# Kernel tuning notes

Measured on AMD Instinct MI355X. Metric: run time of the kernel, lower is better.

## Reference

```python
import jax, jax.numpy as jnp
import numpy as np

B, S, D, E = 4, 2048, 1024, 8
HD = D // E          # per-expert head dim = 128
ROPE = HD // 2       # rotary dims = 64 (32 complex pairs)


def setup_inputs() -> dict:
    key = jax.random.key(0)
    ks = jax.random.split(key, 5)
    x = jax.random.normal(ks[0], (B, S, D), dtype=jnp.float32)
    Wg = jax.random.normal(ks[1], (D, E), dtype=jnp.float32) * 0.02
    Wqkv = jax.random.normal(ks[2], (E, D, 3 * HD), dtype=jnp.float32) * 0.02
    Wff = jax.random.normal(ks[3], (E, HD, D), dtype=jnp.float32) * 0.02
    b_ff = jnp.zeros((D,), dtype=jnp.float32)
    # precompute_freqs_cis(qk_rope_head_dim=ROPE, seqlen=S), theta=10000
    inv = 1.0 / (10000.0 ** (np.arange(0, ROPE, 2, dtype=np.float32) / ROPE))  # [ROPE//2]
    ang = np.arange(S, dtype=np.float32)[:, None] * inv[None, :]               # [S, ROPE//2]
    cos = jnp.asarray(np.cos(ang), dtype=jnp.float32)
    sin = jnp.asarray(np.sin(ang), dtype=jnp.float32)
    return {"x": x, "Wg": Wg, "Wqkv": Wqkv, "Wff": Wff, "b_ff": b_ff, "cos": cos, "sin": sin}


def _apply_rope(x, cos, sin):
    # x: [B,S,E,HD]; rotate the second half (x_pe), keep first half (x_nope), cat (pe, nope)
    b, s, e, hd = x.shape
    x_nope, x_pe = x[..., : hd // 2], x[..., hd // 2 :]
    xr = x_pe.reshape(b, s, e, hd // 4, 2)
    re, im = xr[..., 0], xr[..., 1]
    c = cos[None, :, None, :]
    sn = sin[None, :, None, :]
    rot = jnp.stack([re * c - im * sn, re * sn + im * c], axis=-1).reshape(b, s, e, hd // 2)
    return jnp.concatenate([rot, x_nope], axis=-1)


def reference(x, Wg, Wqkv, Wff, b_ff, cos, sin):
    b, s, d = x.shape
    e, hd = Wqkv.shape[0], Wqkv.shape[2] // 3
    # RoPE on per-expert chunks
    xh = _apply_rope(x.reshape(b, s, e, hd), cos, sin).reshape(b, s, d)
    # SwitchGate: top-1 routing
    probs = jax.nn.softmax(xh @ Wg, axis=-1)            # [b,s,E]
    expert = jnp.argmax(probs, axis=-1)                 # [b,s]
    gate = jnp.max(probs, axis=-1)                      # [b,s]
    # preprocess: per-expert stable gather of routed tokens (capacity = s, padded+masked)
    is_e = expert[None, :, :] == jnp.arange(e)[:, None, None]        # [E,b,s] bool
    order = jnp.argsort(jnp.where(is_e, 0, 1), axis=-1, stable=True)  # [E,b,s] routed-first
    mask_g = jnp.take_along_axis(is_e, order, axis=-1).astype(xh.dtype)  # [E,b,s]
    x_g = jnp.take_along_axis(xh[None], order[..., None], axis=2)    # [E,b,s,d]
    gate_g = jnp.take_along_axis(gate[None], order, axis=2)          # [E,b,s]
    # expert-grouped column-parallel QKV
    qkv = jnp.einsum("ebsd,edf->ebsf", x_g, Wqkv)                    # [E,b,s,3*hd]
    q, k, v = jnp.split(qkv, 3, axis=-1)                             # [E,b,s,hd]
    # grouped sparse attention within each expert's token set
    dot = jnp.einsum("ebqh,ebkh->ebqk", q, k) / jnp.sqrt(jnp.asarray(hd, xh.dtype))
    dot = dot - 1e6 * (1.0 - mask_g[:, :, None, :])
    attn = jax.nn.softmax(dot, axis=-1)
    ctx = jnp.einsum("ebqk,ebkh->ebqh", attn, v)                     # [E,b,s,hd]
    # row-parallel output projection, gate-weighted
    out = jnp.einsum("ebsh,ehd->ebsd", ctx, Wff) + b_ff
    out = out * (gate_g * mask_g)[..., None]
    # scatter_add combine back to [b,s,d]
    outs = jnp.zeros((b, s, d), dtype=xh.dtype)
    outs = outs.at[jnp.arange(b)[None, :, None], order].add(out)
    return outs
```

## Files before the change

kernel.cpp:

```cpp
#include <hip/hip_runtime.h>
#include <math.h>

#define Bn 4
#define Sn 2048
#define Dn 1024
#define En 8
#define HDn 128
#define NG 32
#define MAXT 160
#define MAXN 1024

typedef __attribute__((ext_vector_type(8))) short bf16x8;
typedef __attribute__((ext_vector_type(4))) float f32x4;
typedef unsigned short u16;

__device__ __forceinline__ unsigned bf16_rn(float x) {
  unsigned u = __float_as_uint(x);
  return (u + 0x7fffu + ((u >> 16) & 1u)) >> 16;
}
__device__ __forceinline__ void bsplit(float x, unsigned& hi, unsigned& lo) {
  hi = bf16_rn(x);
  lo = bf16_rn(x - __uint_as_float(hi << 16));
}
__device__ __forceinline__ void gl16(const void* g, void* l) {
  __builtin_amdgcn_global_load_lds(
      (const __attribute__((address_space(1))) void*)g,
      (__attribute__((address_space(3))) void*)l, 16, 0, 0);
}
#define MFMA16(a, b, c) __builtin_amdgcn_mfma_f32_16x16x32_bf16((a), (b), (c), 0, 0, 0)

__device__ __forceinline__ void prep_body(
    const float* __restrict__ W, u16* __restrict__ hiT, u16* __restrict__ loT,
    int Kdim, int Ndim, int e, int k0, int c0, float (*tile)[65])
{
  int t = threadIdx.x;
  int r = t >> 4, cc = (t & 15) << 2;
  const float* src = W + ((size_t)e * Kdim + k0) * Ndim + c0;
#pragma unroll
  for (int i = 0; i < 4; ++i) {
    float4 v = *(const float4*)(src + (size_t)(r + i * 16) * Ndim + cc);
    tile[r + i * 16][cc + 0] = v.x; tile[r + i * 16][cc + 1] = v.y;
    tile[r + i * 16][cc + 2] = v.z; tile[r + i * 16][cc + 3] = v.w;
  }
  __syncthreads();
#pragma unroll
  for (int i = 0; i < 4; ++i) {
    int oc = (t >> 4) + i * 16;
    int ok = (t & 15) << 2;
    float v0 = tile[ok + 0][oc], v1 = tile[ok + 1][oc];
    float v2 = tile[ok + 2][oc], v3 = tile[ok + 3][oc];
    unsigned h0,l0,h1,l1,h2,l2,h3,l3;
    bsplit(v0,h0,l0); bsplit(v1,h1,l1); bsplit(v2,h2,l2); bsplit(v3,h3,l3);
    size_t o = ((size_t)e * Ndim + c0 + oc) * Kdim + k0 + ok;
    *(ushort4*)(hiT + o) = make_ushort4((u16)h0,(u16)h1,(u16)h2,(u16)h3);
    *(ushort4*)(loT + o) = make_ushort4((u16)l0,(u16)l1,(u16)l2,(u16)l3);
  }
}

__global__ __launch_bounds__(256) void k_prologue(
    const float* __restrict__ x, const float* __restrict__ Wg,
    const float* __restrict__ cosT, const float* __restrict__ sinT,
    const float* __restrict__ Wqkv, const float* __restrict__ Wff,
    u16* __restrict__ xh_hi, u16* __restrict__ xh_lo,
    u16* __restrict__ WqT_hi, u16* __restrict__ WqT_lo,
    u16* __restrict__ WfT_hi, u16* __restrict__ WfT_lo,
    int* __restrict__ expertArr, float* __restrict__ gateArr,
    int* __restrict__ done)
{
  __shared__ float tile[64][65];
  int bid = blockIdx.x;
  if (bid == 0 && threadIdx.x == 0) done[0] = 0;
  if (bid < 2048) {
    int wid = threadIdx.x >> 6, l = threadIdx.x & 63;
    int bs = (bid << 2) + wid;
    int s  = bs & (Sn - 1);
    const float* xrow = x + (size_t)bs * Dn;
    float xa[8], xb[8];
#pragma unroll
    for (int d = 0; d < 8; ++d) {
      xa[d] = xrow[d * 128 + l];
      xb[d] = xrow[d * 128 + 64 + l];
    }
    float ce = cosT[s * 32 + (l >> 1)];
    float sn = sinT[s * 32 + (l >> 1)];
    float ve[8];
#pragma unroll
    for (int d = 0; d < 8; ++d) {
      float self = xb[d];
      float part = __shfl_xor(self, 1, 64);
      ve[d] = (l & 1) ? (part * sn + self * ce) : (self * ce - part * sn);
    }
    size_t obase = (size_t)bs * Dn + l;
#pragma unroll
    for (int d = 0; d < 8; ++d) {
      unsigned h0, l0, h1, l1;
      bsplit(ve[d], h0, l0);
      bsplit(xa[d], h1, l1);
      xh_hi[obase + d * 128]      = (u16)h0;
      xh_lo[obase + d * 128]      = (u16)l0;
      xh_hi[obase + d * 128 + 64] = (u16)h1;
      xh_lo[obase + d * 128 + 64] = (u16)l1;
    }

    float pl[8] = {0.f, 0.f, 0.f, 0.f, 0.f, 0.f, 0.f, 0.f};
#pragma unroll
    for (int d = 0; d < 8; ++d) {
      const float* w0 = Wg + (size_t)(d * 128 + l) * En;
      float4 wA = *(const float4*)w0;
      float4 wB = *(const float4*)(w0 + 4);
      float xv = ve[d];
      pl[0] += xv * wA.x; pl[1] += xv * wA.y; pl[2] += xv * wA.z; pl[3] += xv * wA.w;
      pl[4] += xv * wB.x; pl[5] += xv * wB.y; pl[6] += xv * wB.z; pl[7] += xv * wB.w;
      const float* w1 = Wg + (size_t)(d * 128 + 64 + l) * En;
      float4 wC = *(const float4*)w1;
      float4 wD = *(const float4*)(w1 + 4);
      xv = xa[d];
      pl[0] += xv * wC.x; pl[1] += xv * wC.y; pl[2] += xv * wC.z; pl[3] += xv * wC.w;
      pl[4] += xv * wD.x; pl[5] += xv * wD.y; pl[6] += xv * wD.z; pl[7] += xv * wD.w;
    }
#pragma unroll
    for (int off = 1; off < 64; off <<= 1) {
#pragma unroll
      for (int e = 0; e < 8; ++e) pl[e] += __shfl_xor(pl[e], off, 64);
    }
    float m = pl[0]; int be = 0;
#pragma unroll
    for (int e = 1; e < 8; ++e) if (pl[e] > m) { m = pl[e]; be = e; }
    float ss = 0.f;
#pragma unroll
    for (int e = 0; e < 8; ++e) ss += expf(pl[e] - m);
    if (l == 0) {
      expertArr[bs] = be;
      gateArr[bs] = 1.0f / ss;
    }
  } else if (bid < 2048 + 768) {
    int id = bid - 2048;
    int e = id / 96, r2 = id % 96;
    prep_body(Wqkv, WqT_hi, WqT_lo, Dn, 384, e, (r2 / 6) << 6, (r2 % 6) << 6, tile);
  } else {
    int id = bid - 2816;
    int e = id >> 5, r2 = id & 31;
    prep_body(Wff, WfT_hi, WfT_lo, HDn, Dn, e, (r2 >> 4) << 6, (r2 & 15) << 6, tile);
  }
}

__global__ __launch_bounds__(256) void k_route(
    const int* __restrict__ expertArr, int* __restrict__ idx, int* __restrict__ cnt,
    int* __restrict__ tileg, int* __restrict__ tilem, int* __restrict__ ntile,
    int* __restrict__ done)
{
  int g = blockIdx.x;
  int b = g >> 3, e = g & 7;
  int t = threadIdx.x;
  __shared__ int wtot[4];
  __shared__ int base;
  if (t == 0) base = 0;
  __syncthreads();
  for (int c = 0; c < Sn; c += 256) {
    int s = c + t;
    int pred = (expertArr[b * Sn + s] == e) ? 1 : 0;
    unsigned long long mask = __ballot(pred);
    int ln = t & 63, wv = t >> 6;
    int wpre = __popcll(mask & ((1ull << ln) - 1ull));
    if (ln == 63) wtot[wv] = wpre + pred;
    __syncthreads();
    int woff = 0;
    for (int w = 0; w < wv; ++w) woff += wtot[w];
    int tot = wtot[0] + wtot[1] + wtot[2] + wtot[3];
    if (pred) idx[(g << 11) + base + woff + wpre] = s;
    __syncthreads();
    if (t == 0) base += tot;
    __syncthreads();
  }
  if (t == 0) {
    cnt[g] = base;
    __threadfence();
    if (atomicAdd(done, 1) == NG - 1) {
      int tc = 0;
      for (int gg = 0; gg < NG; ++gg) {
        int nn = __hip_atomic_load(&cnt[gg], __ATOMIC_ACQUIRE, __HIP_MEMORY_SCOPE_AGENT);
        for (int m0 = 0; m0 < nn && tc < MAXT; m0 += 64) { tileg[tc] = gg; tilem[tc] = m0; ++tc; }
      }
      ntile[0] = tc;
    }
  }
}

__global__ __launch_bounds__(256) void k_qkv(
    const u16* __restrict__ xh_hi, const u16* __restrict__ xh_lo,
    const u16* __restrict__ WqT_hi, const u16* __restrict__ WqT_lo,
    const int* __restrict__ idx, const int* __restrict__ cnt,
    u16* __restrict__ qkv_hi, u16* __restrict__ qkv_lo,
    u16* __restrict__ vT_hi, u16* __restrict__ vT_lo)
{
  extern __shared__ unsigned char LDS[];
  int bid = blockIdx.x;
  int r8 = bid & 7, q = bid >> 3;
  int g = r8 + ((q & 3) << 3);
  int slot = q >> 2;
  int m0 = (slot >> 1) << 6;
  int n0 = (slot & 1) * 192;
  int n = cnt[g];
  if (m0 >= n) return;
  int b = g >> 3, e = g & 7;
  const int* idxg = idx + (g << 11);
  int t = threadIdx.x;
  int w = t >> 6, l = t & 63;
  int lc = l & 15, lq = l >> 4;

  int srow = t >> 2;
  int sslot = (t & 3) ^ ((srow >> 1) & 3);
  int rgs = m0 + srow; rgs = rgs < n ? rgs : n - 1;
  size_t aoffR = ((size_t)(b * Sn + idxg[rgs])) * Dn + sslot * 8;
  size_t boffR0 = ((size_t)e * 384 + n0 + srow) * Dn + sslot * 8;
  unsigned dst = (unsigned)t << 4;

  f32x4 acc[4][3];
#pragma unroll
  for (int i = 0; i < 4; ++i)
#pragma unroll
    for (int j = 0; j < 3; ++j) acc[i][j] = (f32x4){0.f, 0.f, 0.f, 0.f};

  unsigned off = (unsigned)((lq ^ ((lc >> 1) & 3)) << 4);

#define STAGE(bb, k0)                                                 \
  do {                                                                \
    gl16(xh_hi + aoffR + (k0), LDS + (bb) + dst);                     \
    gl16(xh_lo + aoffR + (k0), LDS + (bb) + 4096 + dst);              \
    gl16(WqT_hi + boffR0 + (k0), LDS + (bb) + 8192 + dst);            \
    gl16(WqT_hi + boffR0 + (size_t)64 * Dn + (k0), LDS + (bb) + 12288 + dst); \
    gl16(WqT_hi + boffR0 + (size_t)128 * Dn + (k0), LDS + (bb) + 16384 + dst);\
    gl16(WqT_lo + boffR0 + (k0), LDS + (bb) + 20480 + dst);           \
    gl16(WqT_lo + boffR0 + (size_t)64 * Dn + (k0), LDS + (bb) + 24576 + dst); \
    gl16(WqT_lo + boffR0 + (size_t)128 * Dn + (k0), LDS + (bb) + 28672 + dst);\
  } while (0)

  STAGE(0, 0);
  asm volatile("s_waitcnt vmcnt(0)" ::: "memory");
  __builtin_amdgcn_s_barrier();
  for (int tt = 0; tt < 32; ++tt) {
    unsigned cur = (tt & 1) ? 32768u : 0u;
    if (tt < 31) {
      STAGE(cur ^ 32768u, (tt + 1) * 32);
      asm volatile("s_waitcnt vmcnt(8)" ::: "memory");
    } else {
      asm volatile("s_waitcnt vmcnt(0)" ::: "memory");
    }
    __builtin_amdgcn_s_barrier();
    bf16x8 ah[4], al[4], bh[3], bl[3];
#pragma unroll
    for (int fi = 0; fi < 4; ++fi) {
      unsigned ab = cur + (unsigned)((fi * 16 + lc) * 64) + off;
      ah[fi] = *(const bf16x8*)(LDS + ab);
      al[fi] = *(const bf16x8*)(LDS + ab + 4096);
    }
#pragma unroll
    for (int fj = 0; fj < 3; ++fj) {
      unsigned bb2 = cur + 8192u + (unsigned)((w * 48 + fj * 16 + lc) * 64) + off;
      bh[fj] = *(const bf16x8*)(LDS + bb2);
      bl[fj] = *(const bf16x8*)(LDS + bb2 + 12288);
    }
    __builtin_amdgcn_s_setprio(1);
#pragma unroll
    for (int fi = 0; fi < 4; ++fi)
#pragma unroll
      for (int fj = 0; fj < 3; ++fj) {
        acc[fi][fj] = MFMA16(ah[fi], bh[fj], acc[fi][fj]);
        acc[fi][fj] = MFMA16(al[fi], bh[fj], acc[fi][fj]);
        acc[fi][fj] = MFMA16(ah[fi], bl[fj], acc[fi][fj]);
      }
    __builtin_amdgcn_s_setprio(0);
    asm volatile("s_waitcnt lgkmcnt(0)" ::: "memory");
    __builtin_amdgcn_sched_barrier(0);
    __builtin_amdgcn_s_barrier();
  }
#undef STAGE

#pragma unroll
  for (int fi = 0; fi < 4; ++fi) {
#pragma unroll
    for (int rr = 0; rr < 4; ++rr) {
      int rg = m0 + fi * 16 + lq * 4 + rr;
      if (rg < n) {
        int tok = idxg[rg];
#pragma unroll
        for (int fj = 0; fj < 3; ++fj) {
          int col = n0 + w * 48 + fj * 16 + lc;
          unsigned h, lo2;
          bsplit(acc[fi][fj][rr], h, lo2);
          if (col < 256) {
            size_t o = (size_t)(b * Sn + tok) * 384 + col;
            qkv_hi[o] = (u16)h; qkv_lo[o] = (u16)lo2;
          } else {
            size_t o = ((size_t)g * HDn + (col - 256)) * MAXN + rg;
            vT_hi[o] = (u16)h; vT_lo[o] = (u16)lo2;
          }
        }
      }
    }
  }
}

__global__ __launch_bounds__(256) void k_attn(
    const u16* __restrict__ qkv_hi, const u16* __restrict__ qkv_lo,
    const u16* __restrict__ vT_hi, const u16* __restrict__ vT_lo,
    const int* __restrict__ idx, const int* __restrict__ cnt,
    const int* __restrict__ tileg, const int* __restrict__ tilem,
    const int* __restrict__ ntile,
    u16* __restrict__ ctx_hi, u16* __restrict__ ctx_lo)
{
  extern __shared__ unsigned char LDS[];
  int tid = blockIdx.x;
  if (tid >= ntile[0]) return;
  int g = tileg[tid], m0 = tilem[tid];
  int n = cnt[g];
  int b = g >> 3;
  const int* idxg = idx + (g << 11);
  int t = threadIdx.x, wid = t >> 6, l = t & 63;
  int lc = l & 15, lq = l >> 4;
  const float scale = 0.08838834764831845f;

  int qrg = m0 + wid * 16 + lc; qrg = qrg < n ? qrg : n - 1;
  size_t qoff = (size_t)(b * Sn + idxg[qrg]) * 384 + lq * 8;
  bf16x8 Qhi[4], Qlo[4];
#pragma unroll
  for (int ks = 0; ks < 4; ++ks) {
    Qhi[ks] = *(const bf16x8*)(qkv_hi + qoff + ks * 32);
    Qlo[ks] = *(const bf16x8*)(qkv_lo + qoff + ks * 32);
  }

  f32x4 acc[8];
#pragma unroll
  for (int i = 0; i < 8; ++i) acc[i] = (f32x4){0.f, 0.f, 0.f, 0.f};
  float m_r[4] = {-1e30f, -1e30f, -1e30f, -1e30f};
  float l_r[4] = {0.f, 0.f, 0.f, 0.f};

  size_t vbase = ((size_t)g * HDn + lc) * MAXN + lq * 8;
  unsigned pbase = 65536u + wid * 4096u;

#define STAGEK(bufb, kc)                                                     \
  do {                                                                       \
    unsigned bb = (bufb);                                                    \
    for (int j = 0; j < 4; ++j) {                                            \
      int c = wid * 4 + j;                                                   \
      int row = (kc) + c * 4 + lq;                                           \
      int rg = row < n ? row : n - 1;                                        \
      int srcslot = lc ^ (((c & 1) << 2) | lq);                              \
      size_t soff = (size_t)(b * Sn + idxg[rg]) * 384 + 128 + srcslot * 8;   \
      gl16(qkv_hi + soff, LDS + bb + c * 1024);                              \
      gl16(qkv_lo + soff, LDS + bb + 16384 + c * 1024);                      \
    }                                                                        \
  } while (0)

  int nt = (n + 63) >> 6;
  STAGEK(0, 0);
  __syncthreads();

  for (int tt = 0; tt < nt; ++tt) {
    unsigned cur = (tt & 1) ? 32768u : 0u;
    if (tt + 1 < nt) STAGEK(cur ^ 32768u, (tt + 1) * 64);
    int kc = tt * 64;

    f32x4 Sf[4];
#pragma unroll
    for (int kf = 0; kf < 4; ++kf) Sf[kf] = (f32x4){0.f, 0.f, 0.f, 0.f};
    __builtin_amdgcn_s_setprio(1);
#pragma unroll
    for (int ks = 0; ks < 4; ++ks) {
#pragma unroll
      for (int kf = 0; kf < 4; ++kf) {
        int row = kf * 16 + lc;
        unsigned byte = cur + row * 256 + ((((ks << 2) | lq) ^ (row & 7)) << 4);
        bf16x8 kh = *(const bf16x8*)(LDS + byte);
        bf16x8 kl = *(const bf16x8*)(LDS + byte + 16384);
        Sf[kf] = MFMA16(Qhi[ks], kh, Sf[kf]);
        Sf[kf] = MFMA16(Qlo[ks], kh, Sf[kf]);
        Sf[kf] = MFMA16(Qhi[ks], kl, Sf[kf]);
      }
    }
    __builtin_amdgcn_s_setprio(0);

    float mloc[4] = {-1e30f, -1e30f, -1e30f, -1e30f};
#pragma unroll
    for (int kf = 0; kf < 4; ++kf) {
#pragma unroll
      for (int r = 0; r < 4; ++r) {
        int key = kc + kf * 16 + lc;
        float s = (key < n) ? Sf[kf][r] * scale : -1e30f;
        Sf[kf][r] = s;
        mloc[r] = fmaxf(mloc[r], s);
      }
    }
#pragma unroll
    for (int off = 1; off < 16; off <<= 1) {
#pragma unroll
      for (int r = 0; r < 4; ++r) mloc[r] = fmaxf(mloc[r], __shfl_xor(mloc[r], off, 64));
    }
    float corr[4], rs[4] = {0.f, 0.f, 0.f, 0.f};
#pragma unroll
    for (int r = 0; r < 4; ++r) {
      float mn = fmaxf(m_r[r], mloc[r]);
      corr[r] = expf(m_r[r] - mn);
      m_r[r] = mn;
    }
#pragma unroll
    for (int kf = 0; kf < 4; ++kf) {
#pragma unroll
      for (int r = 0; r < 4; ++r) {
        float p = expf(Sf[kf][r] - m_r[r]);
        rs[r] += p;
        unsigned ph, plo;
        bsplit(p, ph, plo);
        int prow = (lq << 2) | r;
        int slot = (kf << 1) | (lc >> 3);
        unsigned pb = pbase + prow * 128 + ((slot ^ (prow & 7)) << 4) + ((lc & 7) << 1);
        *(u16*)(LDS + pb) = (u16)ph;
        *(u16*)(LDS + pb + 2048) = (u16)plo;
      }
    }
#pragma unroll
    for (int off = 1; off < 16; off <<= 1) {
#pragma unroll
      for (int r = 0; r < 4; ++r) rs[r] += __shfl_xor(rs[r], off, 64);
    }
#pragma unroll
    for (int r = 0; r < 4; ++r) l_r[r] = l_r[r] * corr[r] + rs[r];
#pragma unroll
    for (int df = 0; df < 8; ++df)
#pragma unroll
      for (int r = 0; r < 4; ++r) acc[df][r] *= corr[r];

#pragma unroll
    for (int ks2 = 0; ks2 < 2; ++ks2) {
      unsigned pr = pbase + lc * 128 + ((((ks2 << 2) | lq) ^ (lc & 7)) << 4);
      bf16x8 pa = *(const bf16x8*)(LDS + pr);
      bf16x8 pl = *(const bf16x8*)(LDS + pr + 2048);
      __builtin_amdgcn_s_setprio(1);
#pragma unroll
      for (int df = 0; df < 8; ++df) {
        size_t vo = vbase + (size_t)(df * 16) * MAXN + kc + ks2 * 32;
        bf16x8 vh = *(const bf16x8*)(vT_hi + vo);
        bf16x8 vl = *(const bf16x8*)(vT_lo + vo);
        acc[df] = MFMA16(pa, vh, acc[df]);
        acc[df] = MFMA16(pl, vh, acc[df]);
        acc[df] = MFMA16(pa, vl, acc[df]);
      }
      __builtin_amdgcn_s_setprio(0);
    }
    __syncthreads();
  }
#undef STAGEK

#pragma unroll
  for (int r = 0; r < 4; ++r) {
    int rg = m0 + wid * 16 + (lq << 2) + r;
    if (rg < n) {
      int tok = idxg[rg];
      float inv = 1.0f / l_r[r];
      size_t o = (size_t)(b * Sn + tok) * HDn + lc;
#pragma unroll
      for (int df = 0; df < 8; ++df) {
        unsigned h, lo2;
        bsplit(acc[df][r] * inv, h, lo2);
        ctx_hi[o + df * 16] = (u16)h;
        ctx_lo[o + df * 16] = (u16)lo2;
      }
    }
  }
}

__global__ __launch_bounds__(256) void k_out(
    const u16* __restrict__ ctx_hi, const u16* __restrict__ ctx_lo,
    const u16* __restrict__ WfT_hi, const u16* __restrict__ WfT_lo,
    const float* __restrict__ bff,
    const int* __restrict__ idx, const int* __restrict__ cnt,
    const int* __restrict__ tileg, const int* __restrict__ tilem,
    const int* __restrict__ ntile,
    const float* __restrict__ gateArr,
    float* __restrict__ out)
{
  int tid = blockIdx.x;
  if (tid >= ntile[0]) return;
  int g = tileg[tid], m0 = tilem[tid];
  int n = cnt[g];
  int b = g >> 3, e = g & 7;
  const int* idxg = idx + (g << 11);
  int t = threadIdx.x, wid = t >> 6, l = t & 63;
  int lc = l & 15, lq = l >> 4;
  int n0 = blockIdx.y * 256 + wid * 64;

  f32x4 acc[4][4];
#pragma unroll
  for (int i = 0; i < 4; ++i)
#pragma unroll
    for (int j = 0; j < 4; ++j) acc[i][j] = (f32x4){0.f, 0.f, 0.f, 0.f};

  size_t aoff[4];
#pragma unroll
  for (int fi = 0; fi < 4; ++fi) {
    int rg = m0 + fi * 16 + lc; rg = rg < n ? rg : n - 1;
    aoff[fi] = ((size_t)(b * Sn + idxg[rg])) * HDn + lq * 8;
  }
  size_t boff[4];
#pragma unroll
  for (int fj = 0; fj < 4; ++fj)
    boff[fj] = ((size_t)e * Dn + n0 + fj * 16 + lc) * HDn + lq * 8;

#pragma unroll
  for (int ks = 0; ks < 4; ++ks) {
    int ko = ks * 32;
    bf16x8 ah[4], al[4], bh[4], bl[4];
#pragma unroll
    for (int fi = 0; fi < 4; ++fi) {
      ah[fi] = *(const bf16x8*)(ctx_hi + aoff[fi] + ko);
      al[fi] = *(const bf16x8*)(ctx_lo + aoff[fi] + ko);
    }
#pragma unroll
    for (int fj = 0; fj < 4; ++fj) {
      bh[fj] = *(const bf16x8*)(WfT_hi + boff[fj] + ko);
      bl[fj] = *(const bf16x8*)(WfT_lo + boff[fj] + ko);
    }
#pragma unroll
    for (int fi = 0; fi < 4; ++fi)
#pragma unroll
      for (int fj = 0; fj < 4; ++fj) {
        acc[fi][fj] = MFMA16(ah[fi], bh[fj], acc[fi][fj]);
        acc[fi][fj] = MFMA16(al[fi], bh[fj], acc[fi][fj]);
        acc[fi][fj] = MFMA16(ah[fi], bl[fj], acc[fi][fj]);
      }
  }

  float bv[4];
#pragma unroll
  for (int fj = 0; fj < 4; ++fj) bv[fj] = bff[n0 + fj * 16 + lc];

#pragma unroll
  for (int fi = 0; fi < 4; ++fi) {
#pragma unroll
    for (int rr = 0; rr < 4; ++rr) {
      int rg = m0 + fi * 16 + lq * 4 + rr;
      if (rg < n) {
        int tok = idxg[rg];
        float gt = gateArr[b * Sn + tok];
        float* orow = out + ((size_t)(b * Sn + tok)) * Dn + n0 + lc;
#pragma unroll
        for (int fj = 0; fj < 4; ++fj)
          orow[fj * 16] = (acc[fi][fj][rr] + bv[fj]) * gt;
      }
    }
  }
}

extern "C" void kernel_launch(void* const* d_in, const int* in_sizes, int n_in,
                              void* d_out, int out_size, void* d_ws, size_t ws_size,
                              hipStream_t stream) {
  const float* x    = (const float*)d_in[0];
  const float* Wg   = (const float*)d_in[1];
  const float* Wqkv = (const float*)d_in[2];
  const float* Wff  = (const float*)d_in[3];
  const float* bff  = (const float*)d_in[4];
  const float* cosT = (const float*)d_in[5];
  const float* sinT = (const float*)d_in[6];
  float* out = (float*)d_out;

  size_t off = 0;
  auto carve = [&](size_t bytes) -> void* {
    void* p = (char*)d_ws + off;
    off += (bytes + 255) & ~(size_t)255;
    return p;
  };
  u16* xh_hi  = (u16*)carve((size_t)Bn * Sn * Dn * 2);
  u16* xh_lo  = (u16*)carve((size_t)Bn * Sn * Dn * 2);
  u16* WqT_hi = (u16*)carve((size_t)En * 384 * Dn * 2);
  u16* WqT_lo = (u16*)carve((size_t)En * 384 * Dn * 2);
  u16* WfT_hi = (u16*)carve((size_t)En * Dn * HDn * 2);
  u16* WfT_lo = (u16*)carve((size_t)En * Dn * HDn * 2);
  u16* qkv_hi = (u16*)carve((size_t)Bn * Sn * 384 * 2);
  u16* qkv_lo = (u16*)carve((size_t)Bn * Sn * 384 * 2);
  u16* vT_hi  = (u16*)carve((size_t)NG * HDn * MAXN * 2);
  u16* vT_lo  = (u16*)carve((size_t)NG * HDn * MAXN * 2);
  u16* ctx_hi = (u16*)carve((size_t)Bn * Sn * HDn * 2);
  u16* ctx_lo = (u16*)carve((size_t)Bn * Sn * HDn * 2);
  float* gateArr = (float*)carve((size_t)Bn * Sn * sizeof(float));
  int*   expertA = (int*)carve((size_t)Bn * Sn * sizeof(int));
  int*   idx     = (int*)carve((size_t)NG * Sn * sizeof(int));
  int*   cnt     = (int*)carve((size_t)NG * sizeof(int));
  int*   tileg   = (int*)carve((size_t)MAXT * sizeof(int));
  int*   tilem   = (int*)carve((size_t)MAXT * sizeof(int));
  int*   ntile   = (int*)carve(256);
  int*   done    = (int*)carve(256);
  (void)ws_size; (void)in_sizes; (void)n_in; (void)out_size;

  hipFuncSetAttribute((const void*)k_attn, hipFuncAttributeMaxDynamicSharedMemorySize, 81920);

  k_prologue<<<dim3(3072), dim3(256), 0, stream>>>(x, Wg, cosT, sinT, Wqkv, Wff,
      xh_hi, xh_lo, WqT_hi, WqT_lo, WfT_hi, WfT_lo, expertA, gateArr, done);
  k_route<<<dim3(NG), dim3(256), 0, stream>>>(expertA, idx, cnt, tileg, tilem, ntile, done);
  k_qkv<<<dim3(384), dim3(256), 65536, stream>>>(xh_hi, xh_lo, WqT_hi, WqT_lo, idx, cnt, qkv_hi, qkv_lo, vT_hi, vT_lo);
  k_attn<<<dim3(MAXT), dim3(256), 81920, stream>>>(qkv_hi, qkv_lo, vT_hi, vT_lo, idx, cnt, tileg, tilem, ntile, ctx_hi, ctx_lo);
  k_out<<<dim3(MAXT, 4), dim3(256), 0, stream>>>(ctx_hi, ctx_lo, WfT_hi, WfT_lo, bff, idx, cnt, tileg, tilem, ntile, gateArr, out);
}
```

Baseline: 169.7 us.

## Split attention into 32-query tiles with 2-wave blocks and finer K pipelining

The attention kernel now uses 32-row query tiles served by 128-thread blocks, with a second tile list built in the routing kernel and a grid of up to 384 blocks. This is meant to spread the roughly 128 attention tiles over more CUs. The K tile shrinks to 32 keys with half the LDS (40KB). Full __syncthreads are replaced by explicit vmcnt/lgkmcnt waits and raw barriers so the next K prefetch can overlap compute. In exchange, K/V traffic and per-block overhead double because each block re-reads all keys for fewer queries, and each loop iteration does less work.

Measured after the change: 182.6 us. 1.08x slower.

```diff
diff --git a/kernel.cpp b/kernel.cpp
--- a/kernel.cpp
+++ b/kernel.cpp
@@ -8,6 +8,7 @@
 #define HDn 128
 #define NG 32
 #define MAXT 160
+#define MAXT2 384
 #define MAXN 1024
 
 typedef __attribute__((ext_vector_type(8))) short bf16x8;
@@ -147,6 +148,7 @@
 __global__ __launch_bounds__(256) void k_route(
     const int* __restrict__ expertArr, int* __restrict__ idx, int* __restrict__ cnt,
     int* __restrict__ tileg, int* __restrict__ tilem, int* __restrict__ ntile,
+    int* __restrict__ tileg2, int* __restrict__ tilem2, int* __restrict__ ntile2,
     int* __restrict__ done)
 {
   int g = blockIdx.x;
@@ -176,12 +178,14 @@
     cnt[g] = base;
     __threadfence();
     if (atomicAdd(done, 1) == NG - 1) {
-      int tc = 0;
+      int tc = 0, tc2 = 0;
       for (int gg = 0; gg < NG; ++gg) {
         int nn = __hip_atomic_load(&cnt[gg], __ATOMIC_ACQUIRE, __HIP_MEMORY_SCOPE_AGENT);
         for (int m0 = 0; m0 < nn && tc < MAXT; m0 += 64) { tileg[tc] = gg; tilem[tc] = m0; ++tc; }
+        for (int m0 = 0; m0 < nn && tc2 < MAXT2; m0 += 32) { tileg2[tc2] = gg; tilem2[tc2] = m0; ++tc2; }
       }
       ntile[0] = tc;
+      ntile2[0] = tc2;
     }
   }
 }
@@ -301,18 +305,18 @@
   }
 }
 
-__global__ __launch_bounds__(256) void k_attn(
+__global__ __launch_bounds__(128) void k_attn(
     const u16* __restrict__ qkv_hi, const u16* __restrict__ qkv_lo,
     const u16* __restrict__ vT_hi, const u16* __restrict__ vT_lo,
     const int* __restrict__ idx, const int* __restrict__ cnt,
-    const int* __restrict__ tileg, const int* __restrict__ tilem,
-    const int* __restrict__ ntile,
+    const int* __restrict__ tileg2, const int* __restrict__ tilem2,
+    const int* __restrict__ ntile2,
     u16* __restrict__ ctx_hi, u16* __restrict__ ctx_lo)
 {
   extern __shared__ unsigned char LDS[];
   int tid = blockIdx.x;
-  if (tid >= ntile[0]) return;
-  int g = tileg[tid], m0 = tilem[tid];
+  if (tid >= ntile2[0]) return;
+  int g = tileg2[tid], m0 = tilem2[tid];
   int n = cnt[g];
   int b = g >> 3;
   const int* idxg = idx + (g << 11);
@@ -336,7 +340,7 @@
   float l_r[4] = {0.f, 0.f, 0.f, 0.f};
 
   size_t vbase = ((size_t)g * HDn + lc) * MAXN + lq * 8;
-  unsigned pbase = 65536u + wid * 4096u;
+  unsigned pbase = 32768u + wid * 4096u;
 
 #define STAGEK(bufb, kc)                                                     \
   do {                                                                       \
@@ -348,31 +352,38 @@
       int srcslot = lc ^ (((c & 1) << 2) | lq);                              \
       size_t soff = (size_t)(b * Sn + idxg[rg]) * 384 + 128 + srcslot * 8;   \
       gl16(qkv_hi + soff, LDS + bb + c * 1024);                              \
-      gl16(qkv_lo + soff, LDS + bb + 16384 + c * 1024);                      \
+      gl16(qkv_lo + soff, LDS + bb + 8192 + c * 1024);                       \
     }                                                                        \
   } while (0)
 
-  int nt = (n + 63) >> 6;
+  int nt = (n + 31) >> 5;
   STAGEK(0, 0);
-  __syncthreads();
+  asm volatile("s_waitcnt vmcnt(0)" ::: "memory");
+  __builtin_amdgcn_s_barrier();
 
   for (int tt = 0; tt < nt; ++tt) {
-    unsigned cur = (tt & 1) ? 32768u : 0u;
-    if (tt + 1 < nt) STAGEK(cur ^ 32768u, (tt + 1) * 64);
-    int kc = tt * 64;
-
-    f32x4 Sf[4];
-#pragma unroll
-    for (int kf = 0; kf < 4; ++kf) Sf[kf] = (f32x4){0.f, 0.f, 0.f, 0.f};
+    unsigned cur = (tt & 1) ? 16384u : 0u;
+    if (tt + 1 < nt) {
+      STAGEK(cur ^ 16384u, (tt + 1) * 32);
+      asm volatile("s_waitcnt vmcnt(8)" ::: "memory");
+    } else {
+      asm volatile("s_waitcnt vmcnt(0)" ::: "memory");
+    }
+    __builtin_amdgcn_s_barrier();
+    int kc = tt * 32;
+
+    f32x4 Sf[2];
+#pragma unroll
+    for (int kf = 0; kf < 2; ++kf) Sf[kf] = (f32x4){0.f, 0.f, 0.f, 0.f};
     __builtin_amdgcn_s_setprio(1);
 #pragma unroll
     for (int ks = 0; ks < 4; ++ks) {
 #pragma unroll
-      for (int kf = 0; kf < 4; ++kf) {
+      for (int kf = 0; kf < 2; ++kf) {
         int row = kf * 16 + lc;
         unsigned byte = cur + row * 256 + ((((ks << 2) | lq) ^ (row & 7)) << 4);
         bf16x8 kh = *(const bf16x8*)(LDS + byte);
-        bf16x8 kl = *(const bf16x8*)(LDS + byte + 16384);
+        bf16x8 kl = *(const bf16x8*)(LDS + byte + 8192);
         Sf[kf] = MFMA16(Qhi[ks], kh, Sf[kf]);
         Sf[kf] = MFMA16(Qlo[ks], kh, Sf[kf]);
         Sf[kf] = MFMA16(Qhi[ks], kl, Sf[kf]);
@@ -382,7 +393,7 @@
 
     float mloc[4] = {-1e30f, -1e30f, -1e30f, -1e30f};
 #pragma unroll
-    for (int kf = 0; kf < 4; ++kf) {
+    for (int kf = 0; kf < 2; ++kf) {
 #pragma unroll
       for (int r = 0; r < 4; ++r) {
         int key = kc + kf * 16 + lc;
@@ -404,7 +415,7 @@
       m_r[r] = mn;
     }
 #pragma unroll
-    for (int kf = 0; kf < 4; ++kf) {
+    for (int kf = 0; kf < 2; ++kf) {
 #pragma unroll
       for (int r = 0; r < 4; ++r) {
         float p = expf(Sf[kf][r] - m_r[r]);
@@ -412,8 +423,8 @@
         unsigned ph, plo;
         bsplit(p, ph, plo);
         int prow = (lq << 2) | r;
-        int slot = (kf << 1) | (lc >> 3);
-        unsigned pb = pbase + prow * 128 + ((slot ^ (prow & 7)) << 4) + ((lc & 7) << 1);
+        int slotp = (kf << 1) | (lc >> 3);
+        unsigned pb = pbase + prow * 128 + ((slotp ^ (prow & 7)) << 4) + ((lc & 7) << 1);
         *(u16*)(LDS + pb) = (u16)ph;
         *(u16*)(LDS + pb + 2048) = (u16)plo;
       }
@@ -430,15 +441,14 @@
 #pragma unroll
       for (int r = 0; r < 4; ++r) acc[df][r] *= corr[r];
 
-#pragma unroll
-    for (int ks2 = 0; ks2 < 2; ++ks2) {
-      unsigned pr = pbase + lc * 128 + ((((ks2 << 2) | lq) ^ (lc & 7)) << 4);
+    {
+      unsigned pr = pbase + lc * 128 + ((lq ^ (lc & 7)) << 4);
       bf16x8 pa = *(const bf16x8*)(LDS + pr);
       bf16x8 pl = *(const bf16x8*)(LDS + pr + 2048);
       __builtin_amdgcn_s_setprio(1);
 #pragma unroll
       for (int df = 0; df < 8; ++df) {
-        size_t vo = vbase + (size_t)(df * 16) * MAXN + kc + ks2 * 32;
+        size_t vo = vbase + (size_t)(df * 16) * MAXN + kc;
         bf16x8 vh = *(const bf16x8*)(vT_hi + vo);
         bf16x8 vl = *(const bf16x8*)(vT_lo + vo);
         acc[df] = MFMA16(pa, vh, acc[df]);
@@ -447,7 +457,9 @@
       }
       __builtin_amdgcn_s_setprio(0);
     }
-    __syncthreads();
+    asm volatile("s_waitcnt lgkmcnt(0)" ::: "memory");
+    __builtin_amdgcn_sched_barrier(0);
+    __builtin_amdgcn_s_barrier();
   }
 #undef STAGEK
 
@@ -588,15 +600,20 @@
   int*   tileg   = (int*)carve((size_t)MAXT * sizeof(int));
   int*   tilem   = (int*)carve((size_t)MAXT * sizeof(int));
   int*   ntile   = (int*)carve(256);
+  int*   tileg2  = (int*)carve((size_t)MAXT2 * sizeof(int));
+  int*   tilem2  = (int*)carve((size_t)MAXT2 * sizeof(int));
+  int*   ntile2  = (int*)carve(256);
   int*   done    = (int*)carve(256);
   (void)ws_size; (void)in_sizes; (void)n_in; (void)out_size;
 
-  hipFuncSetAttribute((const void*)k_attn, hipFuncAttributeMaxDynamicSharedMemorySize, 81920);
+  hipFuncSetAttribute((const void*)k_qkv, hipFuncAttributeMaxDynamicSharedMemorySize, 65536);
+  hipFuncSetAttribute((const void*)k_attn, hipFuncAttributeMaxDynamicSharedMemorySize, 40960);
 
   k_prologue<<<dim3(3072), dim3(256), 0, stream>>>(x, Wg, cosT, sinT, Wqkv, Wff,
       xh_hi, xh_lo, WqT_hi, WqT_lo, WfT_hi, WfT_lo, expertA, gateArr, done);
-  k_route<<<dim3(NG), dim3(256), 0, stream>>>(expertA, idx, cnt, tileg, tilem, ntile, done);
+  k_route<<<dim3(NG), dim3(256), 0, stream>>>(expertA, idx, cnt, tileg, tilem, ntile,
+      tileg2, tilem2, ntile2, done);
   k_qkv<<<dim3(384), dim3(256), 65536, stream>>>(xh_hi, xh_lo, WqT_hi, WqT_lo, idx, cnt, qkv_hi, qkv_lo, vT_hi, vT_lo);
-  k_attn<<<dim3(MAXT), dim3(256), 81920, stream>>>(qkv_hi, qkv_lo, vT_hi, vT_lo, idx, cnt, tileg, tilem, ntile, ctx_hi, ctx_lo);
+  k_attn<<<dim3(MAXT2), dim3(128), 40960, stream>>>(qkv_hi, qkv_lo, vT_hi, vT_lo, idx, cnt, tileg2, tilem2, ntile2, ctx_hi, ctx_lo);
   k_out<<<dim3(MAXT, 4), dim3(256), 0, stream>>>(ctx_hi, ctx_lo, WfT_hi, WfT_lo, bff, idx, cnt, tileg, tilem, ntile, gateArr, out);
 }
```

## Rewrite QKV GEMM with compact 32-row tile list and direct global loads

Applied to the files above, without the earlier changes.

The QKV projection kernel now takes a compact list of 32-row tiles built by the routing kernel. It drops the old fixed grid of 64x192 tiles, which launched many empty blocks, and each block computes all 384 output columns. The LDS double-buffered global_load_lds pipeline is replaced by direct per-lane global vector loads feeding MFMA. The aim is to balance work across blocks and cut the pipeline overhead. The cost is no LDS reuse: each wave loads its B fragments straight from global memory, so global and L2 traffic rises.

New measurement: 260.6 us. +53.6%, slower.

```diff
diff --git a/kernel.cpp b/kernel.cpp
--- a/kernel.cpp
+++ b/kernel.cpp
@@ -8,6 +8,7 @@
 #define HDn 128
 #define NG 32
 #define MAXT 160
+#define MAXT2 384
 #define MAXN 1024
 
 typedef __attribute__((ext_vector_type(8))) short bf16x8;
@@ -147,6 +148,7 @@
 __global__ __launch_bounds__(256) void k_route(
     const int* __restrict__ expertArr, int* __restrict__ idx, int* __restrict__ cnt,
     int* __restrict__ tileg, int* __restrict__ tilem, int* __restrict__ ntile,
+    int* __restrict__ tileg2, int* __restrict__ tilem2, int* __restrict__ ntile2,
     int* __restrict__ done)
 {
   int g = blockIdx.x;
@@ -176,12 +178,14 @@
     cnt[g] = base;
     __threadfence();
     if (atomicAdd(done, 1) == NG - 1) {
-      int tc = 0;
+      int tc = 0, tc2 = 0;
       for (int gg = 0; gg < NG; ++gg) {
         int nn = __hip_atomic_load(&cnt[gg], __ATOMIC_ACQUIRE, __HIP_MEMORY_SCOPE_AGENT);
         for (int m0 = 0; m0 < nn && tc < MAXT; m0 += 64) { tileg[tc] = gg; tilem[tc] = m0; ++tc; }
+        for (int m0 = 0; m0 < nn && tc2 < MAXT2; m0 += 32) { tileg2[tc2] = gg; tilem2[tc2] = m0; ++tc2; }
       }
       ntile[0] = tc;
+      ntile2[0] = tc2;
     }
   }
 }
@@ -190,102 +194,70 @@
     const u16* __restrict__ xh_hi, const u16* __restrict__ xh_lo,
     const u16* __restrict__ WqT_hi, const u16* __restrict__ WqT_lo,
     const int* __restrict__ idx, const int* __restrict__ cnt,
+    const int* __restrict__ tileg2, const int* __restrict__ tilem2,
+    const int* __restrict__ ntile2,
     u16* __restrict__ qkv_hi, u16* __restrict__ qkv_lo,
     u16* __restrict__ vT_hi, u16* __restrict__ vT_lo)
 {
-  extern __shared__ unsigned char LDS[];
-  int bid = blockIdx.x;
-  int r8 = bid & 7, q = bid >> 3;
-  int g = r8 + ((q & 3) << 3);
-  int slot = q >> 2;
-  int m0 = (slot >> 1) << 6;
-  int n0 = (slot & 1) * 192;
+  int tid = blockIdx.x;
+  if (tid >= ntile2[0]) return;
+  int g = tileg2[tid], m0 = tilem2[tid];
   int n = cnt[g];
-  if (m0 >= n) return;
   int b = g >> 3, e = g & 7;
   const int* idxg = idx + (g << 11);
-  int t = threadIdx.x;
-  int w = t >> 6, l = t & 63;
+  int t = threadIdx.x, w = t >> 6, l = t & 63;
   int lc = l & 15, lq = l >> 4;
 
-  int srow = t >> 2;
-  int sslot = (t & 3) ^ ((srow >> 1) & 3);
-  int rgs = m0 + srow; rgs = rgs < n ? rgs : n - 1;
-  size_t aoffR = ((size_t)(b * Sn + idxg[rgs])) * Dn + sslot * 8;
-  size_t boffR0 = ((size_t)e * 384 + n0 + srow) * Dn + sslot * 8;
-  unsigned dst = (unsigned)t << 4;
-
-  f32x4 acc[4][3];
-#pragma unroll
-  for (int i = 0; i < 4; ++i)
-#pragma unroll
-    for (int j = 0; j < 3; ++j) acc[i][j] = (f32x4){0.f, 0.f, 0.f, 0.f};
-
-  unsigned off = (unsigned)((lq ^ ((lc >> 1) & 3)) << 4);
-
-#define STAGE(bb, k0)                                                 \
-  do {                                                                \
-    gl16(xh_hi + aoffR + (k0), LDS + (bb) + dst);                     \
-    gl16(xh_lo + aoffR + (k0), LDS + (bb) + 4096 + dst);              \
-    gl16(WqT_hi + boffR0 + (k0), LDS + (bb) + 8192 + dst);            \
-    gl16(WqT_hi + boffR0 + (size_t)64 * Dn + (k0), LDS + (bb) + 12288 + dst); \
-    gl16(WqT_hi + boffR0 + (size_t)128 * Dn + (k0), LDS + (bb) + 16384 + dst);\
-    gl16(WqT_lo + boffR0 + (k0), LDS + (bb) + 20480 + dst);           \
-    gl16(WqT_lo + boffR0 + (size_t)64 * Dn + (k0), LDS + (bb) + 24576 + dst); \
-    gl16(WqT_lo + boffR0 + (size_t)128 * Dn + (k0), LDS + (bb) + 28672 + dst);\
-  } while (0)
-
-  STAGE(0, 0);
-  asm volatile("s_waitcnt vmcnt(0)" ::: "memory");
-  __builtin_amdgcn_s_barrier();
-  for (int tt = 0; tt < 32; ++tt) {
-    unsigned cur = (tt & 1) ? 32768u : 0u;
-    if (tt < 31) {
-      STAGE(cur ^ 32768u, (tt + 1) * 32);
-      asm volatile("s_waitcnt vmcnt(8)" ::: "memory");
-    } else {
-      asm volatile("s_waitcnt vmcnt(0)" ::: "memory");
-    }
-    __builtin_amdgcn_s_barrier();
-    bf16x8 ah[4], al[4], bh[3], bl[3];
-#pragma unroll
-    for (int fi = 0; fi < 4; ++fi) {
-      unsigned ab = cur + (unsigned)((fi * 16 + lc) * 64) + off;
-      ah[fi] = *(const bf16x8*)(LDS + ab);
-      al[fi] = *(const bf16x8*)(LDS + ab + 4096);
-    }
-#pragma unroll
-    for (int fj = 0; fj < 3; ++fj) {
-      unsigned bb2 = cur + 8192u + (unsigned)((w * 48 + fj * 16 + lc) * 64) + off;
-      bh[fj] = *(const bf16x8*)(LDS + bb2);
-      bl[fj] = *(const bf16x8*)(LDS + bb2 + 12288);
-    }
-    __builtin_amdgcn_s_setprio(1);
-#pragma unroll
-    for (int fi = 0; fi < 4; ++fi)
-#pragma unroll
-      for (int fj = 0; fj < 3; ++fj) {
+  f32x4 acc[2][6];
+#pragma unroll
+  for (int i = 0; i < 2; ++i)
+#pragma unroll
+    for (int j = 0; j < 6; ++j) acc[i][j] = (f32x4){0.f, 0.f, 0.f, 0.f};
+
+  size_t aoff[2];
+#pragma unroll
+  for (int fi = 0; fi < 2; ++fi) {
+    int rg = m0 + fi * 16 + lc; rg = rg < n ? rg : n - 1;
+    aoff[fi] = ((size_t)(b * Sn + idxg[rg])) * Dn + lq * 8;
+  }
+  size_t boff[6];
+#pragma unroll
+  for (int fj = 0; fj < 6; ++fj)
+    boff[fj] = ((size_t)e * 384 + w * 96 + fj * 16 + lc) * Dn + lq * 8;
+
+#pragma unroll 2
+  for (int k0 = 0; k0 < Dn; k0 += 32) {
+    bf16x8 ah[2], al[2], bh[6], bl[6];
+#pragma unroll
+    for (int fi = 0; fi < 2; ++fi) {
+      ah[fi] = *(const bf16x8*)(xh_hi + aoff[fi] + k0);
+      al[fi] = *(const bf16x8*)(xh_lo + aoff[fi] + k0);
+    }
+#pragma unroll
+    for (int fj = 0; fj < 6; ++fj) {
+      bh[fj] = *(const bf16x8*)(WqT_hi + boff[fj] + k0);
+      bl[fj] = *(const bf16x8*)(WqT_lo + boff[fj] + k0);
+    }
+#pragma unroll
+    for (int fi = 0; fi < 2; ++fi)
+#pragma unroll
+      for (int fj = 0; fj < 6; ++fj) {
         acc[fi][fj] = MFMA16(ah[fi], bh[fj], acc[fi][fj]);
         acc[fi][fj] = MFMA16(al[fi], bh[fj], acc[fi][fj]);
         acc[fi][fj] = MFMA16(ah[fi], bl[fj], acc[fi][fj]);
       }
-    __builtin_amdgcn_s_setprio(0);
-    asm volatile("s_waitcnt lgkmcnt(0)" ::: "memory");
-    __builtin_amdgcn_sched_barrier(0);
-    __builtin_amdgcn_s_barrier();
-  }
-#undef STAGE
-
-#pragma unroll
-  for (int fi = 0; fi < 4; ++fi) {
+  }
+
+#pragma unroll
+  for (int fi = 0; fi < 2; ++fi) {
 #pragma unroll
     for (int rr = 0; rr < 4; ++rr) {
       int rg = m0 + fi * 16 + lq * 4 + rr;
       if (rg < n) {
         int tok = idxg[rg];
 #pragma unroll
-        for (int fj = 0; fj < 3; ++fj) {
-          int col = n0 + w * 48 + fj * 16 + lc;
+        for (int fj = 0; fj < 6; ++fj) {
+          int col = w * 96 + fj * 16 + lc;
           unsigned h, lo2;
           bsplit(acc[fi][fj][rr], h, lo2);
           if (col < 256) {
@@ -412,8 +384,8 @@
         unsigned ph, plo;
         bsplit(p, ph, plo);
         int prow = (lq << 2) | r;
-        int slot = (kf << 1) | (lc >> 3);
-        unsigned pb = pbase + prow * 128 + ((slot ^ (prow & 7)) << 4) + ((lc & 7) << 1);
+        int slotp = (kf << 1) | (lc >> 3);
+        unsigned pb = pbase + prow * 128 + ((slotp ^ (prow & 7)) << 4) + ((lc & 7) << 1);
         *(u16*)(LDS + pb) = (u16)ph;
         *(u16*)(LDS + pb + 2048) = (u16)plo;
       }
@@ -588,6 +560,9 @@
   int*   tileg   = (int*)carve((size_t)MAXT * sizeof(int));
   int*   tilem   = (int*)carve((size_t)MAXT * sizeof(int));
   int*   ntile   = (int*)carve(256);
+  int*   tileg2  = (int*)carve((size_t)MAXT2 * sizeof(int));
+  int*   tilem2  = (int*)carve((size_t)MAXT2 * sizeof(int));
+  int*   ntile2  = (int*)carve(256);
   int*   done    = (int*)carve(256);
   (void)ws_size; (void)in_sizes; (void)n_in; (void)out_size;
 
@@ -595,8 +570,10 @@
 
   k_prologue<<<dim3(3072), dim3(256), 0, stream>>>(x, Wg, cosT, sinT, Wqkv, Wff,
       xh_hi, xh_lo, WqT_hi, WqT_lo, WfT_hi, WfT_lo, expertA, gateArr, done);
-  k_route<<<dim3(NG), dim3(256), 0, stream>>>(expertA, idx, cnt, tileg, tilem, ntile, done);
-  k_qkv<<<dim3(384), dim3(256), 65536, stream>>>(xh_hi, xh_lo, WqT_hi, WqT_lo, idx, cnt, qkv_hi, qkv_lo, vT_hi, vT_lo);
+  k_route<<<dim3(NG), dim3(256), 0, stream>>>(expertA, idx, cnt, tileg, tilem, ntile,
+      tileg2, tilem2, ntile2, done);
+  k_qkv<<<dim3(MAXT2), dim3(256), 0, stream>>>(xh_hi, xh_lo, WqT_hi, WqT_lo, idx, cnt,
+      tileg2, tilem2, ntile2, qkv_hi, qkv_lo, vT_hi, vT_lo);
   k_attn<<<dim3(MAXT), dim3(256), 81920, stream>>>(qkv_hi, qkv_lo, vT_hi, vT_lo, idx, cnt, tileg, tilem, ntile, ctx_hi, ctx_lo);
   k_out<<<dim3(MAXT, 4), dim3(256), 0, stream>>>(ctx_hi, ctx_lo, WfT_hi, WfT_lo, bff, idx, cnt, tileg, tilem, ntile, gateArr, out);
 }
```

## Use 8-wave blocks in QKV GEMM and async double-buffer waits in attention

Applied to the files above, without the earlier changes.

The QKV GEMM block grows from 256 to 512 threads, with waves laid out as a 2x4 grid over the 64x192 output tile. Each wave now holds half as many accumulators, and each thread issues 4 instead of 8 global-to-LDS loads per stage. In the attention kernel, the K-tile prefetch now uses explicit vmcnt waits and raw barriers in place of __syncthreads, so the next tile's loads can stay in flight while the current tile is computed. The cost is more waves contending for LDS and barriers. There is also a risk that the vmcnt counts do not match the number of loads outstanding.

After: 172.0 us. No clear change (+1.3%).

```diff
diff --git a/kernel.cpp b/kernel.cpp
--- a/kernel.cpp
+++ b/kernel.cpp
@@ -8,6 +8,7 @@
 #define HDn 128
 #define NG 32
 #define MAXT 160
+#define MAXT2 384
 #define MAXN 1024
 
 typedef __attribute__((ext_vector_type(8))) short bf16x8;
@@ -186,7 +187,7 @@
   }
 }
 
-__global__ __launch_bounds__(256) void k_qkv(
+__global__ __launch_bounds__(512) void k_qkv(
     const u16* __restrict__ xh_hi, const u16* __restrict__ xh_lo,
     const u16* __restrict__ WqT_hi, const u16* __restrict__ WqT_lo,
     const int* __restrict__ idx, const int* __restrict__ cnt,
@@ -205,34 +206,48 @@
   int b = g >> 3, e = g & 7;
   const int* idxg = idx + (g << 11);
   int t = threadIdx.x;
-  int w = t >> 6, l = t & 63;
+  int wid = t >> 6, l = t & 63;
+  int wr = wid >> 2, wc = wid & 3;
   int lc = l & 15, lq = l >> 4;
 
-  int srow = t >> 2;
-  int sslot = (t & 3) ^ ((srow >> 1) & 3);
-  int rgs = m0 + srow; rgs = rgs < n ? rgs : n - 1;
-  size_t aoffR = ((size_t)(b * Sn + idxg[rgs])) * Dn + sslot * 8;
-  size_t boffR0 = ((size_t)e * 384 + n0 + srow) * Dn + sslot * 8;
-  unsigned dst = (unsigned)t << 4;
-
-  f32x4 acc[4][3];
-#pragma unroll
-  for (int i = 0; i < 4; ++i)
+  int ac = t & 255;
+  int arow = ac >> 2;
+  int asl = (ac & 3) ^ ((arow >> 1) & 3);
+  int rga = m0 + arow; rga = rga < n ? rga : n - 1;
+  const u16* Asrc = (t < 256) ? xh_hi : xh_lo;
+  size_t aoffR = ((size_t)(b * Sn + idxg[rga])) * Dn + asl * 8;
+  unsigned adst = (t < 256 ? 0u : 4096u) + ((unsigned)ac << 4);
+  const u16* Bsrc0; const u16* Bsrc1; const u16* Bsrc2;
+  size_t boffR[3];
+  unsigned bdst[3];
+#pragma unroll
+  for (int j = 0; j < 3; ++j) {
+    int c = t + 512 * j;
+    int hi = (c < 768) ? 1 : 0;
+    int bc = hi ? c : c - 768;
+    int brow = bc >> 2;
+    int bsl = (bc & 3) ^ ((brow >> 1) & 3);
+    boffR[j] = ((size_t)e * 384 + n0 + brow) * Dn + bsl * 8;
+    bdst[j] = (hi ? 8192u : 20480u) + ((unsigned)bc << 4);
+    if (j == 0) Bsrc0 = hi ? WqT_hi : WqT_lo;
+    if (j == 1) Bsrc1 = hi ? WqT_hi : WqT_lo;
+    if (j == 2) Bsrc2 = hi ? WqT_hi : WqT_lo;
+  }
+
+  f32x4 acc[2][3];
+#pragma unroll
+  for (int i = 0; i < 2; ++i)
 #pragma unroll
     for (int j = 0; j < 3; ++j) acc[i][j] = (f32x4){0.f, 0.f, 0.f, 0.f};
 
   unsigned off = (unsigned)((lq ^ ((lc >> 1) & 3)) << 4);
 
-#define STAGE(bb, k0)                                                 \
-  do {                                                                \
-    gl16(xh_hi + aoffR + (k0), LDS + (bb) + dst);                     \
-    gl16(xh_lo + aoffR + (k0), LDS + (bb) + 4096 + dst);              \
-    gl16(WqT_hi + boffR0 + (k0), LDS + (bb) + 8192 + dst);            \
-    gl16(WqT_hi + boffR0 + (size_t)64 * Dn + (k0), LDS + (bb) + 12288 + dst); \
-    gl16(WqT_hi + boffR0 + (size_t)128 * Dn + (k0), LDS + (bb) + 16384 + dst);\
-    gl16(WqT_lo + boffR0 + (k0), LDS + (bb) + 20480 + dst);           \
-    gl16(WqT_lo + boffR0 + (size_t)64 * Dn + (k0), LDS + (bb) + 24576 + dst); \
-    gl16(WqT_lo + boffR0 + (size_t)128 * Dn + (k0), LDS + (bb) + 28672 + dst);\
+#define STAGE(bb, k0)                                          \
+  do {                                                         \
+    gl16(Asrc + aoffR + (k0), LDS + (bb) + adst);              \
+    gl16(Bsrc0 + boffR[0] + (k0), LDS + (bb) + bdst[0]);       \
+    gl16(Bsrc1 + boffR[1] + (k0), LDS + (bb) + bdst[1]);       \
+    gl16(Bsrc2 + boffR[2] + (k0), LDS + (bb) + bdst[2]);       \
   } while (0)
 
   STAGE(0, 0);
@@ -242,27 +257,27 @@
     unsigned cur = (tt & 1) ? 32768u : 0u;
     if (tt < 31) {
       STAGE(cur ^ 32768u, (tt + 1) * 32);
-      asm volatile("s_waitcnt vmcnt(8)" ::: "memory");
+      asm volatile("s_waitcnt vmcnt(4)" ::: "memory");
     } else {
       asm volatile("s_waitcnt vmcnt(0)" ::: "memory");
     }
     __builtin_amdgcn_s_barrier();
-    bf16x8 ah[4], al[4], bh[3], bl[3];
-#pragma unroll
-    for (int fi = 0; fi < 4; ++fi) {
-      unsigned ab = cur + (unsigned)((fi * 16 + lc) * 64) + off;
+    bf16x8 ah[2], al[2], bh[3], bl[3];
+#pragma unroll
+    for (int fi = 0; fi < 2; ++fi) {
+      unsigned ab = cur + (unsigned)((wr * 32 + fi * 16 + lc) * 64) + off;
       ah[fi] = *(const bf16x8*)(LDS + ab);
       al[fi] = *(const bf16x8*)(LDS + ab + 4096);
     }
 #pragma unroll
     for (int fj = 0; fj < 3; ++fj) {
-      unsigned bb2 = cur + 8192u + (unsigned)((w * 48 + fj * 16 + lc) * 64) + off;
+      unsigned bb2 = cur + 8192u + (unsigned)((wc * 48 + fj * 16 + lc) * 64) + off;
       bh[fj] = *(const bf16x8*)(LDS + bb2);
       bl[fj] = *(const bf16x8*)(LDS + bb2 + 12288);
     }
     __builtin_amdgcn_s_setprio(1);
 #pragma unroll
-    for (int fi = 0; fi < 4; ++fi)
+    for (int fi = 0; fi < 2; ++fi)
 #pragma unroll
       for (int fj = 0; fj < 3; ++fj) {
         acc[fi][fj] = MFMA16(ah[fi], bh[fj], acc[fi][fj]);
@@ -277,15 +292,15 @@
 #undef STAGE
 
 #pragma unroll
-  for (int fi = 0; fi < 4; ++fi) {
+  for (int fi = 0; fi < 2; ++fi) {
 #pragma unroll
     for (int rr = 0; rr < 4; ++rr) {
-      int rg = m0 + fi * 16 + lq * 4 + rr;
+      int rg = m0 + wr * 32 + fi * 16 + lq * 4 + rr;
       if (rg < n) {
         int tok = idxg[rg];
 #pragma unroll
         for (int fj = 0; fj < 3; ++fj) {
-          int col = n0 + w * 48 + fj * 16 + lc;
+          int col = n0 + wc * 48 + fj * 16 + lc;
           unsigned h, lo2;
           bsplit(acc[fi][fj][rr], h, lo2);
           if (col < 256) {
@@ -354,11 +369,18 @@
 
   int nt = (n + 63) >> 6;
   STAGEK(0, 0);
-  __syncthreads();
+  asm volatile("s_waitcnt vmcnt(0)" ::: "memory");
+  __builtin_amdgcn_s_barrier();
 
   for (int tt = 0; tt < nt; ++tt) {
     unsigned cur = (tt & 1) ? 32768u : 0u;
-    if (tt + 1 < nt) STAGEK(cur ^ 32768u, (tt + 1) * 64);
+    if (tt + 1 < nt) {
+      STAGEK(cur ^ 32768u, (tt + 1) * 64);
+      asm volatile("s_waitcnt vmcnt(8)" ::: "memory");
+    } else {
+      asm volatile("s_waitcnt vmcnt(0)" ::: "memory");
+    }
+    __builtin_amdgcn_s_barrier();
     int kc = tt * 64;
 
     f32x4 Sf[4];
@@ -412,8 +434,8 @@
         unsigned ph, plo;
         bsplit(p, ph, plo);
         int prow = (lq << 2) | r;
-        int slot = (kf << 1) | (lc >> 3);
-        unsigned pb = pbase + prow * 128 + ((slot ^ (prow & 7)) << 4) + ((lc & 7) << 1);
+        int slotp = (kf << 1) | (lc >> 3);
+        unsigned pb = pbase + prow * 128 + ((slotp ^ (prow & 7)) << 4) + ((lc & 7) << 1);
         *(u16*)(LDS + pb) = (u16)ph;
         *(u16*)(LDS + pb + 2048) = (u16)plo;
       }
@@ -447,7 +469,9 @@
       }
       __builtin_amdgcn_s_setprio(0);
     }
-    __syncthreads();
+    asm volatile("s_waitcnt lgkmcnt(0)" ::: "memory");
+    __builtin_amdgcn_sched_barrier(0);
+    __builtin_amdgcn_s_barrier();
   }
 #undef STAGEK
 
@@ -591,12 +615,13 @@
   int*   done    = (int*)carve(256);
   (void)ws_size; (void)in_sizes; (void)n_in; (void)out_size;
 
+  hipFuncSetAttribute((const void*)k_qkv, hipFuncAttributeMaxDynamicSharedMemorySize, 65536);
   hipFuncSetAttribute((const void*)k_attn, hipFuncAttributeMaxDynamicSharedMemorySize, 81920);
 
   k_prologue<<<dim3(3072), dim3(256), 0, stream>>>(x, Wg, cosT, sinT, Wqkv, Wff,
       xh_hi, xh_lo, WqT_hi, WqT_lo, WfT_hi, WfT_lo, expertA, gateArr, done);
   k_route<<<dim3(NG), dim3(256), 0, stream>>>(expertA, idx, cnt, tileg, tilem, ntile, done);
-  k_qkv<<<dim3(384), dim3(256), 65536, stream>>>(xh_hi, xh_lo, WqT_hi, WqT_lo, idx, cnt, qkv_hi, qkv_lo, vT_hi, vT_lo);
+  k_qkv<<<dim3(384), dim3(512), 65536, stream>>>(xh_hi, xh_lo, WqT_hi, WqT_lo, idx, cnt, qkv_hi, qkv_lo, vT_hi, vT_lo);
   k_attn<<<dim3(MAXT), dim3(256), 81920, stream>>>(qkv_hi, qkv_lo, vT_hi, vT_lo, idx, cnt, tileg, tilem, ntile, ctx_hi, ctx_lo);
   k_out<<<dim3(MAXT, 4), dim3(256), 0, stream>>>(ctx_hi, ctx_lo, WfT_hi, WfT_lo, bff, idx, cnt, tileg, tilem, ntile, gateArr, out);
 }
```
